# Kernel tuning notes

Measured on AMD Instinct MI355X. Metric: run time of the kernel, lower is better.

Reference implementation:

```python
import math
import jax, jax.numpy as jnp
import numpy as np

TREE_DEPTH = 4
NUM_NODES = (1 << TREE_DEPTH) - 1  # 15
TAU_MEM = 0.95
TAU_SYN = 0.95
LN_EPS = 1e-5


def _forward(x, W_proj, threshold, node_weights, gamma, beta):
    B, T, D = x.shape
    padded_T = 1 << math.ceil(math.log2(T))
    x_p = jnp.pad(x, ((0, 0), (0, padded_T - T), (0, 0))) if padded_T > T else x

    eff_depth = min(TREE_DEPTH, int(math.log2(padded_T)))
    num_leaves = 1 << eff_depth
    sub_seq = padded_T // num_leaves
    # leaf states: mean over each contiguous chunk -> [B, num_leaves, D]
    leaves = x_p.reshape(B, num_leaves, sub_seq, D).mean(axis=2)

    leaf_start = (1 << (eff_depth - 1)) - 1
    valid_leaves = min(num_leaves, NUM_NODES - leaf_start)
    node_states = jnp.zeros((B, NUM_NODES, D), x.dtype)
    node_states = node_states.at[:, leaf_start:leaf_start + valid_leaves].set(
        leaves[:, :valid_leaves])

    # LIF membrane/synapse buffers, carried across levels within this forward
    v = jnp.zeros((1, 1, D), x.dtype)
    s = jnp.zeros((1, 1, D), x.dtype)

    # bottom-up tree message passing (static, unrolled: eff_depth levels)
    for level in range(eff_depth - 1, -1, -1):
        level_start = (1 << level) - 1
        level_end = min((1 << (level + 1)) - 1, NUM_NODES)
        nodes = np.arange(level_start, level_end)
        left = 2 * nodes + 1
        right = 2 * nodes + 2
        mask = left < NUM_NODES
        if not mask.any():
            continue  # leaf level: children out of range
        nv, lv, rv = nodes[mask], left[mask], right[mask]
        l_st = node_states[:, lv]   # [B, n, D]
        r_st = node_states[:, rv]   # [B, n, D] (full tree -> rv always valid)
        fused = jnp.concatenate([l_st, r_st], axis=-1)  # [B, n, 2D]
        proj = jnp.einsum('bnk,dk->bnd', fused, W_proj)

        # LIF neuron (training-mode math: surrogate * hard spike)
        s_new = TAU_SYN * s + proj                      # broadcast [B,n,D]
        v_new = TAU_MEM * v + s_new - jax.lax.stop_gradient(s_new)
        spike = (v_new >= threshold).astype(x.dtype)
        v_after = v_new - spike * threshold
        surrogate = jax.nn.sigmoid(25.0 * (v_after - threshold))
        spike_out = surrogate * spike
        v = jax.lax.stop_gradient(v_after.mean(axis=(0, 1), keepdims=True))
        s = jax.lax.stop_gradient(s_new.mean(axis=(0, 1), keepdims=True))

        gated = proj * spike_out
        node_states = node_states.at[:, nv].set(gated)

    # per-dim softmax mixture over the 15 tree nodes
    weights = jax.nn.softmax(node_weights, axis=0)             # [N, D]
    mixture = jnp.einsum('nd,bnd->bd', weights, node_states)   # [B, D]

    out = mixture[:, None, :] + x                              # residual, [B,T,D]
    mu = out.mean(axis=-1, keepdims=True)
    var = out.var(axis=-1, keepdims=True)
    out = (out - mu) / jnp.sqrt(var + LN_EPS) * gamma + beta
    return out


def setup_inputs() -> dict:
    key = jax.random.key(0)
    k0, k1, k2 = jax.random.split(key, 3)
    B, T, D = 8, 4096, 1024
    x = jax.random.normal(k0, (B, T, D), dtype=jnp.float32)
    # nn.Linear(2D, D, bias=False): weight [D, 2D]
    W_proj = jax.random.normal(k1, (D, 2 * D), dtype=jnp.float32) / np.sqrt(2 * D).astype(np.float32)
    threshold = jnp.ones((D,), dtype=jnp.float32)        # LIF init: ones
    node_weights = 0.02 * jax.random.normal(k2, (NUM_NODES, D), dtype=jnp.float32)
    gamma = jnp.ones((D,), dtype=jnp.float32)
    beta = jnp.zeros((D,), dtype=jnp.float32)
    return {"x": x, "W_proj": W_proj, "threshold": threshold,
            "node_weights": node_weights, "gamma": gamma, "beta": beta}


def reference(x, W_proj, threshold, node_weights, gamma, beta):
    return _forward(x, W_proj, threshold, node_weights, gamma, beta)
```

## Files before the change

### kernel.cpp

```cpp
#include <hip/hip_runtime.h>

#define Bq 8
#define Tq 4096
#define Dq 1024
#define NNODES 15

typedef float f32x4 __attribute__((ext_vector_type(4)));

__global__ __launch_bounds__(512) void k_leafmix(const float* __restrict__ x,
                                                 const float* __restrict__ nw,
                                                 float* __restrict__ mixture) {
    const int b     = blockIdx.x >> 5;
    const int slice = blockIdx.x & 31;
    const int d0    = slice * 32;
    const int t     = threadIdx.x;
    const int qd    = t & 7;
    const int rg    = t >> 3;
    const int wv    = t >> 6;
    const int lane  = t & 63;

    const float4* xb = (const float4*)(x + (size_t)b * Tq * Dq + d0) + qd;
    float4 acc[8];
#pragma unroll
    for (int l = 0; l < 8; ++l) acc[l] = {0.f, 0.f, 0.f, 0.f};
#pragma unroll
    for (int l = 0; l < 8; ++l) {
#pragma unroll
        for (int j = 0; j < 4; ++j) {
            const int r = rg + 64 * (l * 4 + j);
            const float4 xv = xb[(size_t)r * (Dq / 4)];
            acc[l].x += xv.x; acc[l].y += xv.y;
            acc[l].z += xv.z; acc[l].w += xv.w;
        }
    }
#pragma unroll
    for (int m = 8; m <= 32; m <<= 1) {
#pragma unroll
        for (int l = 0; l < 8; ++l) {
            acc[l].x += __shfl_xor(acc[l].x, m, 64);
            acc[l].y += __shfl_xor(acc[l].y, m, 64);
            acc[l].z += __shfl_xor(acc[l].z, m, 64);
            acc[l].w += __shfl_xor(acc[l].w, m, 64);
        }
    }
    __shared__ float4 lds[8][8][8];
    if (lane < 8) {
#pragma unroll
        for (int l = 0; l < 8; ++l) lds[wv][lane][l] = acc[l];
    }
    __syncthreads();
    __shared__ float lsum[8][8][4];
    if (t < 64) {
        const int q2 = t >> 3, l2 = t & 7;
        float4 a = lds[0][q2][l2];
#pragma unroll
        for (int w = 1; w < 8; ++w) {
            a.x += lds[w][q2][l2].x; a.y += lds[w][q2][l2].y;
            a.z += lds[w][q2][l2].z; a.w += lds[w][q2][l2].w;
        }
        lsum[q2][l2][0] = a.x; lsum[q2][l2][1] = a.y;
        lsum[q2][l2][2] = a.z; lsum[q2][l2][3] = a.w;
    }
    __syncthreads();
    if (t < 32) {
        const int q2 = t >> 2, c = t & 3;
        const int d  = d0 + q2 * 4 + c;
        float v[NNODES];
        float m = -1e30f;
#pragma unroll
        for (int n = 0; n < NNODES; ++n) {
            v[n] = nw[n * Dq + d];
            m = fmaxf(m, v[n]);
        }
        float denom = 0.f;
#pragma unroll
        for (int n = 0; n < NNODES; ++n) {
            v[n] = expf(v[n] - m);
            denom += v[n];
        }
        const float inv_denom = 1.0f / denom;
        float mix = 0.f;
#pragma unroll
        for (int l = 0; l < 8; ++l)
            mix += (v[7 + l] * inv_denom) * (lsum[q2][l][c] * (1.0f / 256.0f));
        mixture[b * Dq + d] = mix;
    }
}

__global__ __launch_bounds__(256) void k_ln(const float* __restrict__ x,
                                            const float* __restrict__ mixture,
                                            const float* __restrict__ gamma,
                                            const float* __restrict__ beta,
                                            float* __restrict__ out) {
    const int wid  = threadIdx.x >> 6;
    const int lane = threadIdx.x & 63;
    const int row  = blockIdx.x * 4 + wid;
    const int b    = row >> 12;
    const float4* xr = (const float4*)(x + (size_t)row * Dq);
    const float4* mr = (const float4*)(mixture + (size_t)b * Dq);
    float4 o[4];
    float sum = 0.f, sq = 0.f;
#pragma unroll
    for (int k = 0; k < 4; ++k) {
        const float4 xv = xr[lane + 64 * k];
        const float4 mv = mr[lane + 64 * k];
        o[k].x = xv.x + mv.x;
        o[k].y = xv.y + mv.y;
        o[k].z = xv.z + mv.z;
        o[k].w = xv.w + mv.w;
        sum += o[k].x + o[k].y + o[k].z + o[k].w;
        sq  += o[k].x * o[k].x + o[k].y * o[k].y + o[k].z * o[k].z + o[k].w * o[k].w;
    }
#pragma unroll
    for (int i = 32; i >= 1; i >>= 1) {
        sum += __shfl_xor(sum, i, 64);
        sq  += __shfl_xor(sq, i, 64);
    }
    const float mu   = sum * (1.0f / 1024.0f);
    const float var  = sq * (1.0f / 1024.0f) - mu * mu;
    const float rstd = rsqrtf(var + 1e-5f);
    f32x4* orow = (f32x4*)(out + (size_t)row * Dq);
#pragma unroll
    for (int k = 0; k < 4; ++k) {
        const float4 gv = ((const float4*)gamma)[lane + 64 * k];
        const float4 bv = ((const float4*)beta)[lane + 64 * k];
        f32x4 r;
        r.x = (o[k].x - mu) * rstd * gv.x + bv.x;
        r.y = (o[k].y - mu) * rstd * gv.y + bv.y;
        r.z = (o[k].z - mu) * rstd * gv.z + bv.z;
        r.w = (o[k].w - mu) * rstd * gv.w + bv.w;
        __builtin_nontemporal_store(r, &orow[lane + 64 * k]);
    }
}

extern "C" void kernel_launch(void* const* d_in, const int* in_sizes, int n_in,
                              void* d_out, int out_size, void* d_ws, size_t ws_size,
                              hipStream_t stream) {
    const float* x     = (const float*)d_in[0];
    const float* nw    = (const float*)d_in[3];
    const float* gamma = (const float*)d_in[4];
    const float* beta  = (const float*)d_in[5];
    float* out = (float*)d_out;

    float* mixture = (float*)d_ws;

    k_leafmix<<<Bq * 32, 512, 0, stream>>>(x, nw, mixture);
    k_ln<<<Bq * Tq / 4, 256, 0, stream>>>(x, mixture, gamma, beta, out);
}
```

Before: 56.05 us.

## Split leaf-mix reduction by time half and stream second half nontemporally

The leaf-mix kernel now splits each batch's time axis into two halves handled by separate blocks over wider 64-column slices. Each block writes a partial mixture, and the layer-norm kernel sums the two partials. The layer-norm kernel also loads rows from the second time half of each batch with nontemporal loads, aiming to keep the first half resident in cache. This adds an extra mixture read per element and relies on the cache retaining the recently read x data between the two kernels.

```diff
diff --git a/kernel.cpp b/kernel.cpp
--- a/kernel.cpp
+++ b/kernel.cpp
@@ -9,62 +9,58 @@
 
 __global__ __launch_bounds__(512) void k_leafmix(const float* __restrict__ x,
                                                  const float* __restrict__ nw,
-                                                 float* __restrict__ mixture) {
-    const int b     = blockIdx.x >> 5;
-    const int slice = blockIdx.x & 31;
-    const int d0    = slice * 32;
+                                                 float* __restrict__ mixpart) {
+    const int blk   = blockIdx.x;
+    const int b     = blk >> 5;
+    const int slice = (blk >> 1) & 15;
+    const int h     = blk & 1;
+    const int d0    = slice * 64;
     const int t     = threadIdx.x;
-    const int qd    = t & 7;
-    const int rg    = t >> 3;
+    const int qd    = t & 15;
     const int wv    = t >> 6;
     const int lane  = t & 63;
+    const int rgl   = lane >> 4;
+    const int rg    = wv * 4 + rgl;
 
-    const float4* xb = (const float4*)(x + (size_t)b * Tq * Dq + d0) + qd;
-    float4 acc[8];
+    const float4* xb = (const float4*)(x + ((size_t)b * Tq + (size_t)h * 1024) * Dq + d0) + qd;
+    float4 acc[4];
 #pragma unroll
-    for (int l = 0; l < 8; ++l) acc[l] = {0.f, 0.f, 0.f, 0.f};
+    for (int l = 0; l < 4; ++l) acc[l] = {0.f, 0.f, 0.f, 0.f};
 #pragma unroll
-    for (int l = 0; l < 8; ++l) {
-#pragma unroll
-        for (int j = 0; j < 4; ++j) {
-            const int r = rg + 64 * (l * 4 + j);
-            const float4 xv = xb[(size_t)r * (Dq / 4)];
-            acc[l].x += xv.x; acc[l].y += xv.y;
-            acc[l].z += xv.z; acc[l].w += xv.w;
-        }
+    for (int k = 0; k < 32; ++k) {
+        const float4 xv = xb[(size_t)(rg + 32 * k) * (Dq / 4)];
+        acc[k >> 3].x += xv.x; acc[k >> 3].y += xv.y;
+        acc[k >> 3].z += xv.z; acc[k >> 3].w += xv.w;
     }
 #pragma unroll
-    for (int m = 8; m <= 32; m <<= 1) {
+    for (int m = 16; m <= 32; m <<= 1)
 #pragma unroll
-        for (int l = 0; l < 8; ++l) {
+        for (int l = 0; l < 4; ++l) {
             acc[l].x += __shfl_xor(acc[l].x, m, 64);
             acc[l].y += __shfl_xor(acc[l].y, m, 64);
             acc[l].z += __shfl_xor(acc[l].z, m, 64);
             acc[l].w += __shfl_xor(acc[l].w, m, 64);
         }
-    }
-    __shared__ float4 lds[8][8][8];
-    if (lane < 8) {
+    __shared__ float lds[8][16][4][4];
+    if (lane < 16) {
 #pragma unroll
-        for (int l = 0; l < 8; ++l) lds[wv][lane][l] = acc[l];
+        for (int l = 0; l < 4; ++l) {
+            lds[wv][lane][l][0] = acc[l].x; lds[wv][lane][l][1] = acc[l].y;
+            lds[wv][lane][l][2] = acc[l].z; lds[wv][lane][l][3] = acc[l].w;
+        }
     }
     __syncthreads();
-    __shared__ float lsum[8][8][4];
     if (t < 64) {
-        const int q2 = t >> 3, l2 = t & 7;
-        float4 a = lds[0][q2][l2];
+        const int d  = d0 + t;
+        const int q2 = t >> 2, c = t & 3;
+        float s[4];
 #pragma unroll
-        for (int w = 1; w < 8; ++w) {
-            a.x += lds[w][q2][l2].x; a.y += lds[w][q2][l2].y;
-            a.z += lds[w][q2][l2].z; a.w += lds[w][q2][l2].w;
+        for (int l = 0; l < 4; ++l) {
+            float a = lds[0][q2][l][c];
+#pragma unroll
+            for (int w = 1; w < 8; ++w) a += lds[w][q2][l][c];
+            s[l] = a;
         }
-        lsum[q2][l2][0] = a.x; lsum[q2][l2][1] = a.y;
-        lsum[q2][l2][2] = a.z; lsum[q2][l2][3] = a.w;
-    }
-    __syncthreads();
-    if (t < 32) {
-        const int q2 = t >> 2, c = t & 3;
-        const int d  = d0 + q2 * 4 + c;
         float v[NNODES];
         float m = -1e30f;
 #pragma unroll
@@ -81,14 +77,14 @@
         const float inv_denom = 1.0f / denom;
         float mix = 0.f;
 #pragma unroll
-        for (int l = 0; l < 8; ++l)
-            mix += (v[7 + l] * inv_denom) * (lsum[q2][l][c] * (1.0f / 256.0f));
-        mixture[b * Dq + d] = mix;
+        for (int l = 0; l < 4; ++l)
+            mix += (v[7 + h * 4 + l] * inv_denom) * (s[l] * (1.0f / 256.0f));
+        mixpart[((size_t)h * Bq + b) * Dq + d] = mix;
     }
 }
 
 __global__ __launch_bounds__(256) void k_ln(const float* __restrict__ x,
-                                            const float* __restrict__ mixture,
+                                            const float* __restrict__ mixpart,
                                             const float* __restrict__ gamma,
                                             const float* __restrict__ beta,
                                             float* __restrict__ out) {
@@ -96,18 +92,23 @@
     const int lane = threadIdx.x & 63;
     const int row  = blockIdx.x * 4 + wid;
     const int b    = row >> 12;
-    const float4* xr = (const float4*)(x + (size_t)row * Dq);
-    const float4* mr = (const float4*)(mixture + (size_t)b * Dq);
+    const bool nt2 = (row >> 11) & 1;
+    const f32x4* xr = (const f32x4*)(x + (size_t)row * Dq);
+    const float4* m0 = (const float4*)(mixpart + (size_t)b * Dq);
+    const float4* m1 = (const float4*)(mixpart + (size_t)(Bq + b) * Dq);
     float4 o[4];
     float sum = 0.f, sq = 0.f;
 #pragma unroll
     for (int k = 0; k < 4; ++k) {
-        const float4 xv = xr[lane + 64 * k];
-        const float4 mv = mr[lane + 64 * k];
-        o[k].x = xv.x + mv.x;
-        o[k].y = xv.y + mv.y;
-        o[k].z = xv.z + mv.z;
-        o[k].w = xv.w + mv.w;
+        f32x4 xv;
+        if (nt2) xv = __builtin_nontemporal_load(&xr[lane + 64 * k]);
+        else     xv = xr[lane + 64 * k];
+        const float4 a0 = m0[lane + 64 * k];
+        const float4 a1 = m1[lane + 64 * k];
+        o[k].x = xv.x + a0.x + a1.x;
+        o[k].y = xv.y + a0.y + a1.y;
+        o[k].z = xv.z + a0.z + a1.z;
+        o[k].w = xv.w + a0.w + a1.w;
         sum += o[k].x + o[k].y + o[k].z + o[k].w;
         sq  += o[k].x * o[k].x + o[k].y * o[k].y + o[k].z * o[k].z + o[k].w * o[k].w;
     }
@@ -142,8 +143,8 @@
     const float* beta  = (const float*)d_in[5];
     float* out = (float*)d_out;
 
-    float* mixture = (float*)d_ws;
+    float* mixpart = (float*)d_ws;
 
-    k_leafmix<<<Bq * 32, 512, 0, stream>>>(x, nw, mixture);
-    k_ln<<<Bq * Tq / 4, 256, 0, stream>>>(x, mixture, gamma, beta, out);
+    k_leafmix<<<Bq * 32, 512, 0, stream>>>(x, nw, mixpart);
+    k_ln<<<Bq * Tq / 4, 256, 0, stream>>>(x, mixpart, gamma, beta, out);
 }
```

Measured after the change: 56.97 us. Within noise of the previous version (+1.6%).
